# Kernel optimization log

Hardware: AMD Instinct MI355X
Metric: run time of the kernel (lower is better)

Reference implementation:

```python
import jax, jax.numpy as jnp
import numpy as np

M_TOKENS, D_IN, D_OUT = 4096, 4096, 16384


def setup_inputs() -> dict:
    key = jax.random.key(0)
    k1, k2, k3, k4 = jax.random.split(key, 4)
    x = jax.random.normal(k1, (M_TOKENS, D_IN), dtype=jnp.float32)
    # pre-quantized int8 weight, stored [K, N] as in qweight_kn
    qweight_kn = jax.random.randint(k2, (D_IN, D_OUT), -127, 128, dtype=jnp.int8)
    # per-output-channel weight dequant scales (float16 buffer, used as fp32 in kernel)
    weight_scales = jax.random.uniform(k3, (D_OUT,), dtype=jnp.float32, minval=1e-3, maxval=2e-2)
    bias = jax.random.normal(k4, (D_OUT,), dtype=jnp.float32) * 0.01
    return {"x": x, "qweight_kn": qweight_kn, "weight_scales": weight_scales, "bias": bias}


def reference(x, qweight_kn, weight_scales, bias):
    target_dtype = x.dtype
    x2 = x.reshape(-1, x.shape[-1])  # [M, K]
    # dynamic per-token (per-row) symmetric quantization
    x_max = jnp.max(jnp.abs(x2), axis=-1, keepdims=True).astype(jnp.float32) + 1e-5
    x_scales = x_max / 127.0  # [M, 1]
    x_int8 = jnp.clip(jnp.round(x2.astype(jnp.float32) / x_scales), -128, 127).astype(jnp.int8)
    acc = jax.lax.dot_general(
        x_int8, qweight_kn,
        dimension_numbers=(((1,), (0,)), ((), ())),
        preferred_element_type=jnp.int32,
    )  # [M, N] int32
    # fused dequant: row act-scale * col weight-scale, plus bias
    c = acc.astype(jnp.float32) * x_scales * weight_scales[None, :].astype(jnp.float32)
    c = c + bias[None, :]
    out = c.astype(jnp.bfloat16)  # kernel stores bf16
    return out.reshape(*x.shape[:-1], -1).astype(target_dtype)
```

## Files before the change

kernel.cpp:

```cpp
#include <hip/hip_runtime.h>
#include <hip/hip_bf16.h>
#include <stdint.h>

typedef int v4i __attribute__((ext_vector_type(4)));

#define GM 4096
#define GN 16384
#define GK 4096
#define BM 256
#define BN 256
#define BK 64
#define NT (GK / BK)

__device__ __forceinline__ void gload16(const void* g, void* l) {
  __builtin_amdgcn_global_load_lds(
      (const __attribute__((address_space(1))) void*)g,
      (__attribute__((address_space(3))) void*)l, 16, 0, 0);
}

__global__ __launch_bounds__(256) void quant_rows(
    const float* __restrict__ x, int8_t* __restrict__ xq2,
    float* __restrict__ xs, int K) {
  const int row = blockIdx.x;
  const int t = threadIdx.x;
  const float4* src = (const float4*)(x + (size_t)row * K) + t * 4;
  float4 v[4];
  float m = 0.f;
#pragma unroll
  for (int i = 0; i < 4; ++i) {
    v[i] = src[i];
    m = fmaxf(m, fmaxf(fmaxf(fabsf(v[i].x), fabsf(v[i].y)),
                       fmaxf(fabsf(v[i].z), fabsf(v[i].w))));
  }
#pragma unroll
  for (int off = 1; off < 64; off <<= 1)
    m = fmaxf(m, __shfl_xor(m, off, 64));
  __shared__ float wmax[4];
  if ((t & 63) == 0) wmax[t >> 6] = m;
  __syncthreads();
  const float gm = fmaxf(fmaxf(wmax[0], wmax[1]), fmaxf(wmax[2], wmax[3]));
  const float scale = (gm + 1e-5f) / 127.0f;
  if (t == 0) xs[row] = scale;
  unsigned packed[4];
#pragma unroll
  for (int i = 0; i < 4; ++i) {
    float fv[4] = {v[i].x, v[i].y, v[i].z, v[i].w};
    unsigned p = 0;
#pragma unroll
    for (int j = 0; j < 4; ++j) {
      int q = (int)rintf(fv[j] / scale);
      q = max(-128, min(127, q));
      p |= (unsigned)(q & 0xff) << (8 * j);
    }
    packed[i] = p;
  }
  const int tm = row >> 8, f = (row >> 4) & 15, fr = row & 15;
  const int kt = t >> 2, kg = t & 3;
  int8_t* dst =
      xq2 + ((((size_t)(tm * 64 + kt) * 16 + f) * 64) + fr + 16 * kg) * 16;
  *(int4*)dst =
      make_int4((int)packed[0], (int)packed[1], (int)packed[2], (int)packed[3]);
}

__global__ __launch_bounds__(256) void transpose_pack(
    const int* __restrict__ W32, int8_t* __restrict__ Wt2, int K, int N) {
  const int t = threadIdx.x;
  const int tn = blockIdx.x;
  const int kt = blockIdx.y;
  const int nq = t & 63;
  const int kg = t >> 6;
  const int n0 = tn * 256 + nq * 4;
  const int kb = kt * 64 + kg * 16;

  v4i r[16];
#pragma unroll
  for (int k = 0; k < 16; ++k)
    r[k] = *(const v4i*)(W32 + (size_t)(kb + k) * N + n0);

  int o[4][4];
#pragma unroll
  for (int i = 0; i < 4; ++i)
#pragma unroll
    for (int j = 0; j < 4; ++j)
      o[i][j] = (r[4 * j + 0][i] & 0xff) | ((r[4 * j + 1][i] & 0xff) << 8) |
                ((r[4 * j + 2][i] & 0xff) << 16) | (r[4 * j + 3][i] << 24);

  int8_t* base = Wt2 + (((size_t)(tn * 64 + kt) * 16 + (nq >> 2)) * 64 +
                        4 * (nq & 3) + 16 * kg) * 16;
#pragma unroll
  for (int i = 0; i < 4; ++i)
    *(v4i*)(base + i * 16) = *(v4i*)&o[i][0];
}

__global__ __launch_bounds__(512, 2) void gemm_i8(
    const int8_t* __restrict__ Xq2, const int8_t* __restrict__ Wt2,
    const float* __restrict__ xs, const float* __restrict__ wsc,
    const float* __restrict__ bias, float* __restrict__ C) {
  __shared__ __align__(16) int8_t lA[2][16384];

  const int t = threadIdx.x;
  const int lane = t & 63;
  const int w = t >> 6;
  const int wr = w >> 2;
  const int wc = w & 3;
  const int fr = lane & 15;
  const int kg = lane >> 4;

  const int bid = blockIdx.x;
  const int xcd = bid & 7;
  const int q = bid >> 3;
  const int tm = q & 15;
  const int tn = xcd * 8 + (q >> 4);
  const size_t rowA0 = (size_t)tm * BM;
  const size_t rowB0 = (size_t)tn * BN;

  const int8_t* aqB = Xq2 + (size_t)tm * 1048576 + w * 2048 + (size_t)lane * 16;
  const int dstO = w * 2048;

#define STAGE(KT, SLOT)                                           \
  {                                                               \
    const int8_t* p = aqB + (size_t)(KT)*16384;                   \
    gload16(p, &lA[(SLOT)][0] + dstO);                            \
    gload16(p + 1024, &lA[(SLOT)][0] + dstO + 1024);              \
  }

  const int8_t* bq = Wt2 + (size_t)tn * 1048576 + wc * 4096 + (size_t)lane * 16;

  v4i acc[8][4] = {};
  v4i areg[2][8], breg[2][4];

#define LD(dst, ptr)                                        \
  asm volatile("global_load_dwordx4 %0, %1, off"            \
               : "=v"(dst)                                  \
               : "v"(ptr)                                   \
               : "memory")

#define LOADB(KT, S)                                        \
  {                                                         \
    const int8_t* bp = bq + (size_t)(KT)*16384;             \
    LD(breg[S][0], bp);                                     \
    LD(breg[S][1], bp + 1024);                              \
    LD(breg[S][2], bp + 2048);                              \
    LD(breg[S][3], bp + 3072);                              \
  }

#define RD_A8(P)                                                            \
  _Pragma("unroll") for (int mi = 0; mi < 8; ++mi) areg[P][mi] =            \
      *(const v4i*)&lA[(P)][(wr * 8 + mi) * 1024 + lane * 16];

#define MFMA_ALL(PB)                                                        \
  __builtin_amdgcn_s_setprio(1);                                            \
  _Pragma("unroll") for (int mi = 0; mi < 8; ++mi)                          \
      _Pragma("unroll") for (int nj = 0; nj < 4; ++nj)                      \
          acc[mi][nj] = __builtin_amdgcn_mfma_i32_16x16x64_i8(              \
              areg[PB][mi], breg[PB][nj], acc[mi][nj], 0, 0, 0);            \
  __builtin_amdgcn_s_setprio(0);

#define SB __builtin_amdgcn_sched_barrier(0)

#define BODY(T, P)                                                            \
  {                                                                           \
       \
      \
                                  \
    asm volatile("s_waitcnt vmcnt(4)" ::: "memory");                          \
    __builtin_amdgcn_s_barrier();                                             \
    STAGE(((T) + 1) & (NT - 1), ((P) ^ 1));                                   \
    SB;                                                                       \
    RD_A8(P);                                                                 \
    SB;                                                                       \
    MFMA_ALL((P) ^ 1);      \
    asm volatile("s_waitcnt lgkmcnt(0)" ::: "memory");   \
    SB;                                                                       \
    LOADB(((T) + 1) & (NT - 1), ((P) ^ 1));      \
    SB;                                                                       \
  }

  STAGE(0, 0);
  STAGE(1, 1);
  LOADB(0, 0);
  LOADB(1, 1);
  asm volatile("s_waitcnt vmcnt(0)" ::: "memory");
  __builtin_amdgcn_s_barrier();
  RD_A8(0);
  asm volatile("s_waitcnt lgkmcnt(0)" ::: "memory");
  SB;

  BODY(1, 1);
  for (int kt = 2; kt < NT; kt += 2) {
    BODY(kt, 0);
    BODY(kt + 1, 1);
  }
  asm volatile("s_waitcnt vmcnt(0) lgkmcnt(0)" ::: "memory");
  SB;
  MFMA_ALL(1);

#pragma unroll
  for (int nj = 0; nj < 4; ++nj) {
    const int col_l = wc * 64 + nj * 16 + fr;
    const float wsv = wsc[rowB0 + col_l];
    const float bv = bias[rowB0 + col_l];
#pragma unroll
    for (int mi = 0; mi < 8; ++mi) {
#pragma unroll
      for (int r = 0; r < 4; ++r) {
        const size_t row = rowA0 + wr * 128 + mi * 16 + kg * 4 + r;
        const float f = (float)acc[mi][nj][r] * xs[row] * wsv + bv;
        C[row * GN + rowB0 + col_l] = __bfloat162float(__float2bfloat16(f));
      }
    }
  }
}

extern "C" void kernel_launch(void* const* d_in, const int* in_sizes, int n_in,
                              void* d_out, int out_size, void* d_ws, size_t ws_size,
                              hipStream_t stream) {
  const int M = GM, K = GK, N = GN;
  const float* x = (const float*)d_in[0];
  const int* W32 = (const int*)d_in[1];
  const float* wsc = (const float*)d_in[2];
  const float* bias = (const float*)d_in[3];
  float* out = (float*)d_out;

  float* xs = (float*)d_ws;
  int8_t* Xq2 = (int8_t*)d_ws + 16384;
  int8_t* Wt2 = (int8_t*)d_ws + 16384 + (size_t)M * K;

  transpose_pack<<<dim3(N / 256, K / 64), 256, 0, stream>>>(W32, Wt2, K, N);
  quant_rows<<<M, 256, 0, stream>>>(x, Xq2, xs, K);
  gemm_i8<<<dim3((M / BM) * (N / BN)), 512, 0, stream>>>(Xq2, Wt2, xs, wsc, bias,
                                                         out);
}
```

Before: 416.7 us.

## Stage B tiles through LDS and deepen pipeline to four slots

The B (weight) tile is no longer loaded straight into registers with global loads. It is now staged into LDS with global_load_lds, like A, and both operands use a 4-slot LDS ring that processes two K-steps per barrier. This removes the per-wave duplicated direct global loads of B and amortizes barriers over two K tiles. The cost is 128KB of LDS per block, which likely prevents two blocks per CU despite the launch bounds, and a full vmcnt(0) wait each iteration.

New measurement: 460.5 us. +10.5%, slower.

```diff
diff --git a/kernel.cpp b/kernel.cpp
--- a/kernel.cpp
+++ b/kernel.cpp
@@ -96,7 +96,8 @@
     const int8_t* __restrict__ Xq2, const int8_t* __restrict__ Wt2,
     const float* __restrict__ xs, const float* __restrict__ wsc,
     const float* __restrict__ bias, float* __restrict__ C) {
-  __shared__ __align__(16) int8_t lA[2][16384];
+  __shared__ __align__(16) int8_t lA[4][16384];
+  __shared__ __align__(16) int8_t lB[4][16384];
 
   const int t = threadIdx.x;
   const int lane = t & 63;
@@ -115,85 +116,79 @@
   const size_t rowB0 = (size_t)tn * BN;
 
   const int8_t* aqB = Xq2 + (size_t)tm * 1048576 + w * 2048 + (size_t)lane * 16;
+  const int8_t* bqB = Wt2 + (size_t)tn * 1048576 + w * 2048 + (size_t)lane * 16;
   const int dstO = w * 2048;
 
-#define STAGE(KT, SLOT)                                           \
+#define STAGE_A(KT, SL)                                           \
   {                                                               \
     const int8_t* p = aqB + (size_t)(KT)*16384;                   \
-    gload16(p, &lA[(SLOT)][0] + dstO);                            \
-    gload16(p + 1024, &lA[(SLOT)][0] + dstO + 1024);              \
-  }
-
-  const int8_t* bq = Wt2 + (size_t)tn * 1048576 + wc * 4096 + (size_t)lane * 16;
+    gload16(p, &lA[(SL)][0] + dstO);                              \
+    gload16(p + 1024, &lA[(SL)][0] + dstO + 1024);                \
+  }
+#define STAGE_B(KT, SL)                                           \
+  {                                                               \
+    const int8_t* p = bqB + (size_t)(KT)*16384;                   \
+    gload16(p, &lB[(SL)][0] + dstO);                              \
+    gload16(p + 1024, &lB[(SL)][0] + dstO + 1024);                \
+  }
 
   v4i acc[8][4] = {};
   v4i areg[2][8], breg[2][4];
 
-#define LD(dst, ptr)                                        \
-  asm volatile("global_load_dwordx4 %0, %1, off"            \
-               : "=v"(dst)                                  \
-               : "v"(ptr)                                   \
-               : "memory")
-
-#define LOADB(KT, S)                                        \
-  {                                                         \
-    const int8_t* bp = bq + (size_t)(KT)*16384;             \
-    LD(breg[S][0], bp);                                     \
-    LD(breg[S][1], bp + 1024);                              \
-    LD(breg[S][2], bp + 2048);                              \
-    LD(breg[S][3], bp + 3072);                              \
-  }
-
-#define RD_A8(P)                                                            \
-  _Pragma("unroll") for (int mi = 0; mi < 8; ++mi) areg[P][mi] =            \
-      *(const v4i*)&lA[(P)][(wr * 8 + mi) * 1024 + lane * 16];
-
-#define MFMA_ALL(PB)                                                        \
+#define RD_A8(SL, BK_)                                                      \
+  _Pragma("unroll") for (int mi = 0; mi < 8; ++mi) areg[BK_][mi] =          \
+      *(const v4i*)&lA[(SL)][(wr * 8 + mi) * 1024 + lane * 16];
+#define RD_B4(SL, BK_)                                                      \
+  _Pragma("unroll") for (int nj = 0; nj < 4; ++nj) breg[BK_][nj] =          \
+      *(const v4i*)&lB[(SL)][(wc * 4 + nj) * 1024 + lane * 16];
+
+#define MFMA_ALL(BK_)                                                       \
   __builtin_amdgcn_s_setprio(1);                                            \
   _Pragma("unroll") for (int mi = 0; mi < 8; ++mi)                          \
       _Pragma("unroll") for (int nj = 0; nj < 4; ++nj)                      \
           acc[mi][nj] = __builtin_amdgcn_mfma_i32_16x16x64_i8(              \
-              areg[PB][mi], breg[PB][nj], acc[mi][nj], 0, 0, 0);            \
+              areg[BK_][mi], breg[BK_][nj], acc[mi][nj], 0, 0, 0);          \
   __builtin_amdgcn_s_setprio(0);
 
 #define SB __builtin_amdgcn_sched_barrier(0)
 
-#define BODY(T, P)                                                            \
+#define BODY(T, SL0, SL1, SS0, SS1, DO_PREV)                                  \
   {                                                                           \
-       \
-      \
-                                  \
-    asm volatile("s_waitcnt vmcnt(4)" ::: "memory");                          \
-    __builtin_amdgcn_s_barrier();                                             \
-    STAGE(((T) + 1) & (NT - 1), ((P) ^ 1));                                   \
-    SB;                                                                       \
-    RD_A8(P);                                                                 \
-    SB;                                                                       \
-    MFMA_ALL((P) ^ 1);      \
-    asm volatile("s_waitcnt lgkmcnt(0)" ::: "memory");   \
-    SB;                                                                       \
-    LOADB(((T) + 1) & (NT - 1), ((P) ^ 1));      \
-    SB;                                                                       \
-  }
-
-  STAGE(0, 0);
-  STAGE(1, 1);
-  LOADB(0, 0);
-  LOADB(1, 1);
-  asm volatile("s_waitcnt vmcnt(0)" ::: "memory");
-  __builtin_amdgcn_s_barrier();
-  RD_A8(0);
-  asm volatile("s_waitcnt lgkmcnt(0)" ::: "memory");
-  SB;
-
-  BODY(1, 1);
-  for (int kt = 2; kt < NT; kt += 2) {
-    BODY(kt, 0);
-    BODY(kt + 1, 1);
-  }
+    asm volatile("s_waitcnt vmcnt(0)" ::: "memory");  \
+    __builtin_amdgcn_s_barrier();     \
+    STAGE_A(((T) + 2) & (NT - 1), SS0);                                       \
+    STAGE_A(((T) + 3) & (NT - 1), SS1);                                       \
+    STAGE_B(((T) + 2) & (NT - 1), SS0);                                       \
+    STAGE_B(((T) + 3) & (NT - 1), SS1);                                       \
+    SB;                                                                       \
+    RD_A8(SL0, 0);                                                            \
+    RD_B4(SL0, 0);                                                            \
+    SB;                                                                       \
+    if (DO_PREV) { MFMA_ALL(1) }  \
+    asm volatile("s_waitcnt lgkmcnt(0)" ::: "memory");       \
+    SB;                                                                       \
+    RD_A8(SL1, 1);                                                            \
+    RD_B4(SL1, 1);                                                            \
+    SB;                                                                       \
+    MFMA_ALL(0)                                                   \
+    asm volatile("s_waitcnt lgkmcnt(0)" ::: "memory");  \
+    SB;                            \
+  }
+
+  STAGE_A(0, 0);
+  STAGE_A(1, 1);
+  STAGE_B(0, 0);
+  STAGE_B(1, 1);
+
+  BODY(0, 0, 1, 2, 3, 0);
+  for (int kt = 2; kt < NT - 2; kt += 4) {
+    BODY(kt, 2, 3, 0, 1, 1);
+    BODY(kt + 2, 0, 1, 2, 3, 1);
+  }
+  BODY(NT - 2, 2, 3, 0, 1, 1);
   asm volatile("s_waitcnt vmcnt(0) lgkmcnt(0)" ::: "memory");
   SB;
-  MFMA_ALL(1);
+  MFMA_ALL(1)
 
 #pragma unroll
   for (int nj = 0; nj < 4; ++nj) {
```

## Switch int8 GEMM to 32x32x32 MFMA with matching operand packing layout

Applied to the files above, without the earlier changes.

Replaces the 16x16x64 i8 MFMA tiles with 32x32x32 i8 MFMA. The A and B pack kernels and the LDS/register fragment indexing are reorganized into 32-row by 32-k sub-blocks to match. Each wave now holds 4x2 accumulators of 16 ints instead of 8x4 of 4, with each 64-deep k step split into two 32-deep MFMAs. The goal is higher MFMA throughput per instruction and fewer operand reads. The cost is a changed epilogue row mapping and possible LDS bank-conflict or register-pressure changes.

Result: no change. 424.9 us (+2.0%).

```diff
diff --git a/kernel.cpp b/kernel.cpp
--- a/kernel.cpp
+++ b/kernel.cpp
@@ -3,6 +3,7 @@
 #include <stdint.h>
 
 typedef int v4i __attribute__((ext_vector_type(4)));
+typedef int v16i __attribute__((ext_vector_type(16)));
 
 #define GM 4096
 #define GN 16384
@@ -54,10 +55,10 @@
     }
     packed[i] = p;
   }
-  const int tm = row >> 8, f = (row >> 4) & 15, fr = row & 15;
-  const int kt = t >> 2, kg = t & 3;
-  int8_t* dst =
-      xq2 + ((((size_t)(tm * 64 + kt) * 16 + f) * 64) + fr + 16 * kg) * 16;
+  const int tm = row >> 8, f = (row >> 5) & 7, l31 = row & 31;
+  const int kt = t >> 2, s = (t >> 1) & 1, h = t & 1;
+  int8_t* dst = xq2 + (size_t)(tm * 64 + kt) * 16384 + (f * 2 + s) * 1024 +
+                (l31 + 32 * h) * 16;
   *(int4*)dst =
       make_int4((int)packed[0], (int)packed[1], (int)packed[2], (int)packed[3]);
 }
@@ -85,8 +86,9 @@
       o[i][j] = (r[4 * j + 0][i] & 0xff) | ((r[4 * j + 1][i] & 0xff) << 8) |
                 ((r[4 * j + 2][i] & 0xff) << 16) | (r[4 * j + 3][i] << 24);
 
-  int8_t* base = Wt2 + (((size_t)(tn * 64 + kt) * 16 + (nq >> 2)) * 64 +
-                        4 * (nq & 3) + 16 * kg) * 16;
+  const int f = nq >> 3, s = kg >> 1, h = kg & 1;
+  int8_t* base = Wt2 + (size_t)(tn * 64 + kt) * 16384 + (f * 2 + s) * 1024 +
+                 ((nq & 7) * 4 + 32 * h) * 16;
 #pragma unroll
   for (int i = 0; i < 4; ++i)
     *(v4i*)(base + i * 16) = *(v4i*)&o[i][0];
@@ -103,8 +105,8 @@
   const int w = t >> 6;
   const int wr = w >> 2;
   const int wc = w & 3;
-  const int fr = lane & 15;
-  const int kg = lane >> 4;
+  const int l31 = lane & 31;
+  const int h = lane >> 5;
 
   const int bid = blockIdx.x;
   const int xcd = bid & 7;
@@ -117,17 +119,18 @@
   const int8_t* aqB = Xq2 + (size_t)tm * 1048576 + w * 2048 + (size_t)lane * 16;
   const int dstO = w * 2048;
 
-#define STAGE(KT, SLOT)                                           \
+#define STAGE(KT, SL)                                             \
   {                                                               \
     const int8_t* p = aqB + (size_t)(KT)*16384;                   \
-    gload16(p, &lA[(SLOT)][0] + dstO);                            \
-    gload16(p + 1024, &lA[(SLOT)][0] + dstO + 1024);              \
-  }
-
-  const int8_t* bq = Wt2 + (size_t)tn * 1048576 + wc * 4096 + (size_t)lane * 16;
-
-  v4i acc[8][4] = {};
-  v4i areg[2][8], breg[2][4];
+    gload16(p, &lA[(SL)][0] + dstO);                              \
+    gload16(p + 1024, &lA[(SL)][0] + dstO + 1024);                \
+  }
+
+  const int8_t* bq = Wt2 + (size_t)tn * 1048576 + (wc * 2) * 2048 +
+                     (size_t)lane * 16;
+
+  v16i acc[4][2] = {};
+  v4i areg[2][4][2], breg[2][2][2];
 
 #define LD(dst, ptr)                                        \
   asm volatile("global_load_dwordx4 %0, %1, off"            \
@@ -135,41 +138,41 @@
                : "v"(ptr)                                   \
                : "memory")
 
-#define LOADB(KT, S)                                        \
+#define LOADB(KT, BKr)                                      \
   {                                                         \
     const int8_t* bp = bq + (size_t)(KT)*16384;             \
-    LD(breg[S][0], bp);                                     \
-    LD(breg[S][1], bp + 1024);                              \
-    LD(breg[S][2], bp + 2048);                              \
-    LD(breg[S][3], bp + 3072);                              \
-  }
-
-#define RD_A8(P)                                                            \
-  _Pragma("unroll") for (int mi = 0; mi < 8; ++mi) areg[P][mi] =            \
-      *(const v4i*)&lA[(P)][(wr * 8 + mi) * 1024 + lane * 16];
-
-#define MFMA_ALL(PB)                                                        \
+    LD(breg[BKr][0][0], bp);                                \
+    LD(breg[BKr][0][1], bp + 1024);                         \
+    LD(breg[BKr][1][0], bp + 2048);                         \
+    LD(breg[BKr][1][1], bp + 3072);                         \
+  }
+
+#define RD_A8(SL, BKr)                                                      \
+  _Pragma("unroll") for (int mi = 0; mi < 4; ++mi)                          \
+      _Pragma("unroll") for (int s = 0; s < 2; ++s)                         \
+          areg[BKr][mi][s] = *(const v4i*)&lA[(SL)][                        \
+              (((wr * 4 + mi) * 2) + s) * 1024 + lane * 16];
+
+#define MFMA_ALL(BKr)                                                       \
   __builtin_amdgcn_s_setprio(1);                                            \
-  _Pragma("unroll") for (int mi = 0; mi < 8; ++mi)                          \
-      _Pragma("unroll") for (int nj = 0; nj < 4; ++nj)                      \
-          acc[mi][nj] = __builtin_amdgcn_mfma_i32_16x16x64_i8(              \
-              areg[PB][mi], breg[PB][nj], acc[mi][nj], 0, 0, 0);            \
+  _Pragma("unroll") for (int mi = 0; mi < 4; ++mi)                          \
+      _Pragma("unroll") for (int nj = 0; nj < 2; ++nj)                      \
+          _Pragma("unroll") for (int s = 0; s < 2; ++s)                     \
+              acc[mi][nj] = __builtin_amdgcn_mfma_i32_32x32x32_i8(          \
+                  areg[BKr][mi][s], breg[BKr][nj][s], acc[mi][nj], 0, 0, 0);\
   __builtin_amdgcn_s_setprio(0);
 
 #define SB __builtin_amdgcn_sched_barrier(0)
 
 #define BODY(T, P)                                                            \
   {                                                                           \
-       \
-      \
-                                  \
-    asm volatile("s_waitcnt vmcnt(4)" ::: "memory");                          \
-    __builtin_amdgcn_s_barrier();                                             \
+    asm volatile("s_waitcnt vmcnt(4)" ::: "memory");     \
+    __builtin_amdgcn_s_barrier();    \
     STAGE(((T) + 1) & (NT - 1), ((P) ^ 1));                                   \
     SB;                                                                       \
-    RD_A8(P);                                                                 \
-    SB;                                                                       \
-    MFMA_ALL((P) ^ 1);      \
+    RD_A8(P, P);                                                              \
+    SB;                                                                       \
+    MFMA_ALL((P) ^ 1)             \
     asm volatile("s_waitcnt lgkmcnt(0)" ::: "memory");   \
     SB;                                                                       \
     LOADB(((T) + 1) & (NT - 1), ((P) ^ 1));      \
@@ -182,7 +185,7 @@
   LOADB(1, 1);
   asm volatile("s_waitcnt vmcnt(0)" ::: "memory");
   __builtin_amdgcn_s_barrier();
-  RD_A8(0);
+  RD_A8(0, 0);
   asm volatile("s_waitcnt lgkmcnt(0)" ::: "memory");
   SB;
 
@@ -193,18 +196,19 @@
   }
   asm volatile("s_waitcnt vmcnt(0) lgkmcnt(0)" ::: "memory");
   SB;
-  MFMA_ALL(1);
-
-#pragma unroll
-  for (int nj = 0; nj < 4; ++nj) {
-    const int col_l = wc * 64 + nj * 16 + fr;
+  MFMA_ALL(1)
+
+#pragma unroll
+  for (int nj = 0; nj < 2; ++nj) {
+    const int col_l = wc * 64 + nj * 32 + l31;
     const float wsv = wsc[rowB0 + col_l];
     const float bv = bias[rowB0 + col_l];
 #pragma unroll
-    for (int mi = 0; mi < 8; ++mi) {
-#pragma unroll
-      for (int r = 0; r < 4; ++r) {
-        const size_t row = rowA0 + wr * 128 + mi * 16 + kg * 4 + r;
+    for (int mi = 0; mi < 4; ++mi) {
+#pragma unroll
+      for (int r = 0; r < 16; ++r) {
+        const size_t row =
+            rowA0 + wr * 128 + mi * 32 + (r & 3) + 8 * (r >> 2) + 4 * h;
         const float f = (float)acc[mi][nj][r] * xs[row] * wsv + bv;
         C[row * GN + rowB0 + col_l] = __bfloat162float(__float2bfloat16(f));
       }
```
